# Kernel tuning notes

Hardware: AMD Instinct MI355X
Metric: run time of the kernel (lower is better)

The kernel has to match this reference:

```python
import jax, jax.numpy as jnp
import numpy as np

D_MODEL = 128
D_EDGE = 64


def setup_inputs() -> dict:
    key = jax.random.key(0)
    ks = jax.random.split(key, 12)
    B, N, E = 4, 50000, 600000
    x = jax.random.normal(ks[0], (B, N, D_MODEL), dtype=jnp.float32)
    edge_index = jax.random.randint(ks[1], (2, E), 0, N, dtype=jnp.int64)
    e_emb = jax.random.normal(ks[2], (E, D_EDGE), dtype=jnp.float32)
    batch_index = jax.random.randint(ks[3], (E,), 0, B, dtype=jnp.int64)
    s = 1.0 / np.sqrt(D_MODEL)
    se = 1.0 / np.sqrt(D_EDGE)
    Wq = jax.random.normal(ks[4], (D_MODEL, D_MODEL), dtype=jnp.float32) * s
    bq = jnp.zeros((D_MODEL,), dtype=jnp.float32)
    Wk = jax.random.normal(ks[5], (D_MODEL, D_MODEL), dtype=jnp.float32) * s
    bk = jnp.zeros((D_MODEL,), dtype=jnp.float32)
    Wv = jax.random.normal(ks[6], (D_MODEL, D_MODEL), dtype=jnp.float32) * s
    bv = jnp.zeros((D_MODEL,), dtype=jnp.float32)
    Wew = jax.random.normal(ks[7], (D_EDGE, D_MODEL), dtype=jnp.float32) * se
    bew = jnp.zeros((D_MODEL,), dtype=jnp.float32)
    Wev = jax.random.normal(ks[8], (D_EDGE, D_MODEL), dtype=jnp.float32) * se
    bev = jnp.zeros((D_MODEL,), dtype=jnp.float32)
    Wa = jax.random.normal(ks[9], (D_MODEL, 1), dtype=jnp.float32) * s
    return {"x": x, "edge_index": edge_index, "e_emb": e_emb,
            "batch_index": batch_index, "n_heads": 8,
            "Wq": Wq, "bq": bq, "Wk": Wk, "bk": bk, "Wv": Wv, "bv": bv,
            "Wew": Wew, "bew": bew, "Wev": Wev, "bev": bev, "Wa": Wa}


def reference(x, edge_index, e_emb, batch_index, n_heads,
              Wq, bq, Wk, bk, Wv, bv, Wew, bew, Wev, bev, Wa):
    B, N, d = x.shape
    d_h = d // n_heads
    Q = x @ Wq + bq          # [B, N, d]
    K = x @ Wk + bk
    V = x @ Wv + bv
    Ew = e_emb @ Wew + bew   # [E, d]
    Ev = e_emb @ Wev + bev
    src, dst = edge_index[0], edge_index[1]
    q_src = Q[batch_index, src, :]   # [E, d] gathers
    k_dst = K[batch_index, dst, :]
    v_dst = V[batch_index, dst, :]
    att_raw = q_src + k_dst + Ew
    att_logit = (att_raw @ Wa)[:, 0] / np.sqrt(d_h).astype(np.float32)
    att_exp = jnp.exp(att_logit)     # [E]
    group = batch_index * N + dst
    att_sum = jax.ops.segment_sum(att_exp, group, num_segments=B * N)
    alpha = att_exp / (att_sum[group] + 1e-9)
    msg = alpha[:, None] * (v_dst + Ev)          # [E, d]
    group_src = batch_index * N + src
    out_flat = jax.ops.segment_sum(msg, group_src, num_segments=B * N)
    return out_flat.reshape(B, N, d)
```

## Files before the change

kernel.cpp:

```cpp
#include <hip/hip_runtime.h>

#define DM 128
#define DE 64

static constexpr int kB = 4;
static constexpr int kN = 50000;
static constexpr int kE = 600000;
static constexpr int kNodes = kB * kN;

static constexpr size_t OFF_V    = 0;
static constexpr size_t OFF_T    = OFF_V + (size_t)kNodes * DM;
static constexpr size_t OFF_QA   = OFF_T + (size_t)kNodes * DE;
static constexpr size_t OFF_KA   = OFF_QA + kNodes;
static constexpr size_t OFF_ASUM = OFF_KA + kNodes;
static constexpr size_t OFF_CNT  = OFF_ASUM + kNodes;
static constexpr size_t OFF_AEXP = OFF_CNT + kNodes;
static constexpr size_t OFF_OFFS = OFF_AEXP + kE;
static constexpr size_t OFF_POS  = OFF_OFFS + kNodes;
static constexpr size_t OFF_BSUM = OFF_POS + kE;
static constexpr size_t OFF_BPRE = OFF_BSUM + 1024;
static constexpr size_t OFF_REC  = OFF_BPRE + 1024;
static constexpr size_t OFF_WQA  = OFF_REC + (size_t)kE * 4;
static constexpr size_t OFF_WKA  = OFF_WQA + DM;
static constexpr size_t OFF_WEWA = OFF_WKA + DM;
static constexpr size_t OFF_CB   = OFF_WEWA + DE;
static constexpr size_t OFF_WTH  = OFF_CB + 4;
static constexpr size_t OFF_WTL  = OFF_WTH + 8192;

static constexpr int kScanBlocks = (kNodes + 255) / 256;

typedef __attribute__((ext_vector_type(8))) short s8;
typedef __attribute__((ext_vector_type(4))) float f4;

__device__ inline void split2(float f, unsigned short& h, unsigned short& lo) {
  unsigned u = __float_as_uint(f);
  unsigned r = u + 0x7FFFu + ((u >> 16) & 1u);
  h = (unsigned short)(r >> 16);
  float fh = __uint_as_float((unsigned)h << 16);
  float d = f - fh;
  unsigned u2 = __float_as_uint(d);
  unsigned r2 = u2 + 0x7FFFu + ((u2 >> 16) & 1u);
  lo = (unsigned short)(r2 >> 16);
}

__global__ void k0_combine(const float* __restrict__ Wq, const float* __restrict__ Wk,
                           const float* __restrict__ Wew, const float* __restrict__ Wa,
                           const float* __restrict__ bq, const float* __restrict__ bk,
                           const float* __restrict__ bew, float* __restrict__ ws) {
  int t = threadIdx.x;
  if (t < DM) {
    float a = 0.f;
    for (int j = 0; j < DM; ++j) a += Wq[t * DM + j] * Wa[j];
    ws[OFF_WQA + t] = a;
  } else if (t < 2 * DM) {
    int i = t - DM;
    float a = 0.f;
    for (int j = 0; j < DM; ++j) a += Wk[i * DM + j] * Wa[j];
    ws[OFF_WKA + i] = a;
  } else if (t < 2 * DM + DE) {
    int i = t - 2 * DM;
    float a = 0.f;
    for (int j = 0; j < DM; ++j) a += Wew[i * DM + j] * Wa[j];
    ws[OFF_WEWA + i] = a;
  }
  if (t == 0) {
    float a = 0.f;
    for (int j = 0; j < DM; ++j) a += (bq[j] + bk[j] + bew[j]) * Wa[j];
    ws[OFF_CB] = a;
  }
}

__global__ __launch_bounds__(256) void k0b_wsplit(const float* __restrict__ Wv,
                                                  float* __restrict__ ws) {
  int idx = blockIdx.x * 256 + threadIdx.x;
  int j = idx & 127, k = idx >> 7;
  float w = Wv[k * DM + j];
  unsigned short hi, lo;
  split2(w, hi, lo);
  int kc = k & 31;
  int kp = (k & ~31) | (((kc >> 2) & 3) << 3) | ((kc >> 4) << 2) | (kc & 3);
  ((short*)(ws + OFF_WTH))[j * 128 + kp] = (short)hi;
  ((short*)(ws + OFF_WTL))[j * 128 + kp] = (short)lo;
}

__global__ __launch_bounds__(512) void k1_node(const float* __restrict__ x,
                                               const float* __restrict__ bv,
                                               float* __restrict__ ws) {
  __shared__ short xh[128][128];
  __shared__ short xl[128][128];
  __shared__ short wh[128][128];
  __shared__ short wl[128][128];
  const int t = threadIdx.x;
  const int row0 = blockIdx.x * 128;

  const short* wtgh = (const short*)(ws + OFF_WTH);
  const short* wtgl = (const short*)(ws + OFF_WTL);
  #pragma unroll
  for (int i = 0; i < 4; ++i) {
    int idx = t + i * 512;
    int j = idx >> 4;
    int c8 = (idx & 15) * 8;
    int col = (((c8 >> 3) ^ (j & 7)) << 3);
    *(int4*)&wh[j][col] = *(const int4*)(wtgh + j * 128 + c8);
    *(int4*)&wl[j][col] = *(const int4*)(wtgl + j * 128 + c8);
  }

  #pragma unroll
  for (int i = 0; i < 8; ++i) {
    int idx = t + i * 512;
    int r = idx >> 5;
    int c4 = (idx & 31) * 4;
    int rg = row0 + r; if (rg > kNodes - 1) rg = kNodes - 1;
    float4 v = *(const float4*)(x + (size_t)rg * DM + c4);
    unsigned short h0, h1, h2, h3, l0, l1, l2, l3;
    split2(v.x, h0, l0); split2(v.y, h1, l1);
    split2(v.z, h2, l2); split2(v.w, h3, l3);
    int kc = c4 & 31;
    int cp = (c4 & ~31) | (((kc >> 2) & 3) << 3) | ((kc >> 4) << 2);
    int col = ((((cp >> 3) ^ (r & 7)) << 3)) | (cp & 7);
    *(short4*)&xh[r][col] = make_short4((short)h0, (short)h1, (short)h2, (short)h3);
    *(short4*)&xl[r][col] = make_short4((short)l0, (short)l1, (short)l2, (short)l3);
  }

  if (t < 256) {
    int r = t & 127;
    int rg = row0 + r;
    if (rg < kNodes) {
      const float* wvec = (t < 128) ? (ws + OFF_WQA) : (ws + OFF_WKA);
      const float* xr = x + (size_t)rg * DM;
      float a = 0.f;
      #pragma unroll
      for (int k = 0; k < DM; k += 4) {
        float4 xv = *(const float4*)(xr + k);
        float4 wv = *(const float4*)(wvec + k);
        a += xv.x * wv.x + xv.y * wv.y + xv.z * wv.z + xv.w * wv.w;
      }
      ((t < 128) ? (ws + OFF_QA) : (ws + OFF_KA))[rg] = a;
    }
  }

  __syncthreads();

  const int l = t & 63;
  const int wid = t >> 6;
  const int wr = wid >> 1;
  const int wc = wid & 1;
  const int lrow = l & 15;
  const int lg = l >> 4;

  f4 acc[2][4];
  #pragma unroll
  for (int i = 0; i < 2; ++i)
    #pragma unroll
    for (int j = 0; j < 4; ++j) acc[i][j] = (f4){0.f, 0.f, 0.f, 0.f};

  #pragma unroll
  for (int ks = 0; ks < 4; ++ks) {
    s8 ah[2], al[2], bh[4], bl[4];
    #pragma unroll
    for (int i = 0; i < 2; ++i) {
      int r = wr * 32 + i * 16 + lrow;
      int col = (((ks * 4 + lg) ^ (r & 7)) << 3);
      ah[i] = *(const s8*)&xh[r][col];
      al[i] = *(const s8*)&xl[r][col];
    }
    #pragma unroll
    for (int j = 0; j < 4; ++j) {
      int r = wc * 64 + j * 16 + lrow;
      int col = (((ks * 4 + lg) ^ (r & 7)) << 3);
      bh[j] = *(const s8*)&wh[r][col];
      bl[j] = *(const s8*)&wl[r][col];
    }
    #pragma unroll
    for (int i = 0; i < 2; ++i)
      #pragma unroll
      for (int j = 0; j < 4; ++j) {
        acc[i][j] = __builtin_amdgcn_mfma_f32_16x16x32_bf16(ah[i], bh[j], acc[i][j], 0, 0, 0);
        acc[i][j] = __builtin_amdgcn_mfma_f32_16x16x32_bf16(ah[i], bl[j], acc[i][j], 0, 0, 0);
        acc[i][j] = __builtin_amdgcn_mfma_f32_16x16x32_bf16(al[i], bh[j], acc[i][j], 0, 0, 0);
      }
  }

  float* V = ws + OFF_V;
  #pragma unroll
  for (int i = 0; i < 2; ++i) {
    int rb = row0 + wr * 32 + i * 16 + lg * 4;
    #pragma unroll
    for (int j = 0; j < 4; ++j) {
      int colj = wc * 64 + j * 16 + lrow;
      float bvv = bv[colj];
      #pragma unroll
      for (int q = 0; q < 4; ++q) {
        int rr = rb + q;
        if (rr < kNodes) V[(size_t)rr * DM + colj] = acc[i][j][q] + bvv;
      }
    }
  }
}

__global__ __launch_bounds__(256) void k2_edge1(const int* __restrict__ ei,
                                                const int* __restrict__ bidx,
                                                const float* __restrict__ eemb,
                                                float* __restrict__ ws) {
  __shared__ float wewa_s[DE];
  __shared__ float cb_s;
  int t = threadIdx.x;
  if (t < DE) wewa_s[t] = ws[OFF_WEWA + t];
  if (t == DE) cb_s = ws[OFF_CB];
  __syncthreads();
  int e = blockIdx.x * 256 + t;
  if (e >= kE) return;
  int s = ei[e];
  int d = ei[kE + e];
  int b = bidx[e];
  const float4* emb = (const float4*)(eemb + (size_t)e * DE);
  float a = 0.f;
  #pragma unroll
  for (int i = 0; i < 16; ++i) {
    float4 v = emb[i];
    a += v.x * wewa_s[i * 4] + v.y * wewa_s[i * 4 + 1] +
         v.z * wewa_s[i * 4 + 2] + v.w * wewa_s[i * 4 + 3];
  }
  float logit = (ws[OFF_QA + b * kN + s] + ws[OFF_KA + b * kN + d] + a + cb_s) * 0.25f;
  float ex = __expf(logit);
  ws[OFF_AEXP + e] = ex;
  unsafeAtomicAdd(&ws[OFF_ASUM + b * kN + d], ex);
  int* wsi = (int*)ws;
  int gs = b * kN + s;
  wsi[OFF_POS + e] = atomicAdd(&wsi[OFF_CNT + gs], 1);
}

__global__ __launch_bounds__(256) void k_scan1(float* __restrict__ ws) {
  __shared__ int sh[256];
  int* wsi = (int*)ws;
  const int tid = threadIdx.x;
  const int i = blockIdx.x * 256 + tid;
  int v = (i < kNodes) ? wsi[OFF_CNT + i] : 0;
  int acc = v;
  sh[tid] = acc;
  __syncthreads();
  #pragma unroll
  for (int ofs = 1; ofs < 256; ofs <<= 1) {
    int add = (tid >= ofs) ? sh[tid - ofs] : 0;
    __syncthreads();
    acc += add;
    sh[tid] = acc;
    __syncthreads();
  }
  if (i < kNodes) wsi[OFF_OFFS + i] = acc - v;
  if (tid == 255) wsi[OFF_BSUM + blockIdx.x] = acc;
}

__global__ __launch_bounds__(1024) void k_scan2(float* __restrict__ ws) {
  __shared__ int sh[1024];
  int* wsi = (int*)ws;
  const int tid = threadIdx.x;
  int v = (tid < kScanBlocks) ? wsi[OFF_BSUM + tid] : 0;
  int acc = v;
  sh[tid] = acc;
  __syncthreads();
  for (int ofs = 1; ofs < 1024; ofs <<= 1) {
    int add = (tid >= ofs) ? sh[tid - ofs] : 0;
    __syncthreads();
    acc += add;
    sh[tid] = acc;
    __syncthreads();
  }
  wsi[OFF_BPRE + tid] = acc - v;
}

__global__ __launch_bounds__(256) void k_fill(const int* __restrict__ ei,
                                              const int* __restrict__ bidx,
                                              float* __restrict__ ws) {
  int e = blockIdx.x * 256 + threadIdx.x;
  if (e >= kE) return;
  int s = ei[e];
  int d = ei[kE + e];
  int b = bidx[e];
  int gs = b * kN + s;
  int gd = b * kN + d;
  const int* wsi = (const int*)ws;
  float alpha = ws[OFF_AEXP + e] / (ws[OFF_ASUM + gd] + 1e-9f);
  int p = wsi[OFF_OFFS + gs] + wsi[OFF_BPRE + (gs >> 8)] + wsi[OFF_POS + e];
  float4 r;
  r.x = alpha;
  r.y = __int_as_float(gd);
  r.z = __int_as_float(e);
  r.w = 0.f;
  ((float4*)(ws + OFF_REC))[p] = r;
}

__global__ __launch_bounds__(256) void k3_gather(const float* __restrict__ eemb,
                                                 const float* __restrict__ bev,
                                                 float* __restrict__ ws,
                                                 float* __restrict__ out) {
  const int lane = threadIdx.x & 63;
  const int g = (blockIdx.x * 256 + threadIdx.x) >> 6;
  if (g >= kNodes) return;
  const int* wsi = (const int*)ws;
  const float* V = ws + OFF_V;
  float* T = ws + OFF_T;
  const float4* rec = (const float4*)(ws + OFF_REC);
  const float bev0 = bev[lane];
  const float bev1 = bev[64 + lane];

  const int start = wsi[OFF_OFFS + g] + wsi[OFF_BPRE + (g >> 8)];
  const int deg = wsi[OFF_CNT + g];
  float o0 = 0.f, o1 = 0.f, tac = 0.f, ss = 0.f;
  for (int base = 0; base < deg; base += 4) {
    const int rem = deg - base;
    const int c1 = (rem > 1) ? 1 : 0;
    const int c2 = (rem > 2) ? 2 : c1;
    const int c3 = (rem > 3) ? 3 : c2;
    float4 r0 = rec[start + base];
    float4 r1 = rec[start + base + c1];
    float4 r2 = rec[start + base + c2];
    float4 r3 = rec[start + base + c3];
    float a0 = r0.x;
    float a1 = (rem > 1) ? r1.x : 0.f;
    float a2 = (rem > 2) ? r2.x : 0.f;
    float a3 = (rem > 3) ? r3.x : 0.f;
    const size_t gd0 = (size_t)__float_as_int(r0.y) * DM;
    const size_t gd1 = (size_t)__float_as_int(r1.y) * DM;
    const size_t gd2 = (size_t)__float_as_int(r2.y) * DM;
    const size_t gd3 = (size_t)__float_as_int(r3.y) * DM;
    const size_t e0 = (size_t)__float_as_int(r0.z) * DE;
    const size_t e1 = (size_t)__float_as_int(r1.z) * DE;
    const size_t e2 = (size_t)__float_as_int(r2.z) * DE;
    const size_t e3 = (size_t)__float_as_int(r3.z) * DE;
    float v00 = V[gd0 + lane],      v01 = V[gd1 + lane];
    float v02 = V[gd2 + lane],      v03 = V[gd3 + lane];
    float v10 = V[gd0 + 64 + lane], v11 = V[gd1 + 64 + lane];
    float v12 = V[gd2 + 64 + lane], v13 = V[gd3 + 64 + lane];
    float m0 = eemb[e0 + lane],     m1 = eemb[e1 + lane];
    float m2 = eemb[e2 + lane],     m3 = eemb[e3 + lane];
    o0 += a0 * v00 + a1 * v01 + a2 * v02 + a3 * v03;
    o1 += a0 * v10 + a1 * v11 + a2 * v12 + a3 * v13;
    tac += a0 * m0 + a1 * m1 + a2 * m2 + a3 * m3;
    ss += a0 + a1 + a2 + a3;
  }
  out[(size_t)g * DM + lane] = o0 + ss * bev0;
  out[(size_t)g * DM + 64 + lane] = o1 + ss * bev1;
  T[(size_t)g * DE + lane] = tac;
}

__global__ __launch_bounds__(256) void k4_wev(const float* __restrict__ Wev,
                                              float* __restrict__ ws,
                                              float* __restrict__ out) {
  __shared__ float ts[64][68];
  __shared__ float wes[64][132];
  const int t = threadIdx.x;
  const int row0 = blockIdx.x * 64;
  const float* T = ws + OFF_T;

  const float4* tg = (const float4*)(T + (size_t)row0 * DE);
  #pragma unroll
  for (int i = 0; i < 4; ++i) {
    int idx = t + i * 256;
    int r = idx >> 4, c = (idx & 15) * 4;
    *(float4*)&ts[r][c] = tg[idx];
  }
  const float4* wg = (const float4*)Wev;
  #pragma unroll
  for (int i = 0; i < 8; ++i) {
    int idx = t + i * 256;
    int r = idx >> 5, c = (idx & 31) * 4;
    *(float4*)&wes[r][c] = wg[idx];
  }
  __syncthreads();

  const int tx = t & 15, ty = t >> 4;
  const int j0 = tx * 8, r0 = ty * 4;
  float acc[4][8];
  #pragma unroll
  for (int i = 0; i < 4; ++i)
    #pragma unroll
    for (int j = 0; j < 8; ++j) acc[i][j] = 0.f;

  #pragma unroll
  for (int kk = 0; kk < DE; kk += 4) {
    float xv[4][4];
    #pragma unroll
    for (int i = 0; i < 4; ++i) {
      float4 tmp = *(const float4*)&ts[r0 + i][kk];
      xv[i][0] = tmp.x; xv[i][1] = tmp.y; xv[i][2] = tmp.z; xv[i][3] = tmp.w;
    }
    #pragma unroll
    for (int d = 0; d < 4; ++d) {
      float4 w0 = *(const float4*)&wes[kk + d][j0];
      float4 w1 = *(const float4*)&wes[kk + d][j0 + 4];
      float wj[8] = {w0.x, w0.y, w0.z, w0.w, w1.x, w1.y, w1.z, w1.w};
      #pragma unroll
      for (int i = 0; i < 4; ++i)
        #pragma unroll
        for (int j = 0; j < 8; ++j) acc[i][j] += xv[i][d] * wj[j];
    }
  }

  #pragma unroll
  for (int i = 0; i < 4; ++i) {
    size_t g = (size_t)(row0 + r0 + i);
    float4 o0 = *(const float4*)&out[g * DM + j0];
    float4 o1 = *(const float4*)&out[g * DM + j0 + 4];
    o0.x += acc[i][0]; o0.y += acc[i][1]; o0.z += acc[i][2]; o0.w += acc[i][3];
    o1.x += acc[i][4]; o1.y += acc[i][5]; o1.z += acc[i][6]; o1.w += acc[i][7];
    *(float4*)&out[g * DM + j0] = o0;
    *(float4*)&out[g * DM + j0 + 4] = o1;
  }
}

extern "C" void kernel_launch(void* const* d_in, const int* in_sizes, int n_in,
                              void* d_out, int out_size, void* d_ws, size_t ws_size,
                              hipStream_t stream) {
  const float* x    = (const float*)d_in[0];
  const int*   ei   = (const int*)d_in[1];
  const float* eemb = (const float*)d_in[2];
  const int*   bidx = (const int*)d_in[3];
  const float* Wq  = (const float*)d_in[5];
  const float* bq  = (const float*)d_in[6];
  const float* Wk  = (const float*)d_in[7];
  const float* bk  = (const float*)d_in[8];
  const float* Wv  = (const float*)d_in[9];
  const float* bv  = (const float*)d_in[10];
  const float* Wew = (const float*)d_in[11];
  const float* bew = (const float*)d_in[12];
  const float* Wev = (const float*)d_in[13];
  const float* bev = (const float*)d_in[14];
  const float* Wa  = (const float*)d_in[15];
  float* ws  = (float*)d_ws;
  float* out = (float*)d_out;

  hipMemsetAsync(ws + OFF_ASUM, 0, (size_t)2 * kNodes * sizeof(float), stream);

  k0_combine<<<1, 320, 0, stream>>>(Wq, Wk, Wew, Wa, bq, bk, bew, ws);
  k0b_wsplit<<<64, 256, 0, stream>>>(Wv, ws);
  k1_node<<<(kNodes + 127) / 128, 512, 0, stream>>>(x, bv, ws);
  k2_edge1<<<(kE + 255) / 256, 256, 0, stream>>>(ei, bidx, eemb, ws);
  k_scan1<<<kScanBlocks, 256, 0, stream>>>(ws);
  k_scan2<<<1, 1024, 0, stream>>>(ws);
  k_fill<<<(kE + 255) / 256, 256, 0, stream>>>(ei, bidx, ws);
  k3_gather<<<kNodes / 4, 256, 0, stream>>>(eemb, bev, ws, out);
  k4_wev<<<kNodes / 64, 256, 0, stream>>>(Wev, ws, out);
}
```

Measured before the change: 639.6 us.

## Fuse Wev projection into gather kernel via register-resident bf16 weights

Removes the separate k4_wev GEMM kernel and the T intermediate round-trip. The gather kernel now keeps Wev in registers as packed bf16 pairs, broadcasts each lane's accumulated edge-embedding sum with readlane, and applies the 64x128 projection before writing out. It also switches to a persistent grid-stride loop with 4096 blocks so the weight load is amortized. The cost is 64 extra VGPRs per thread, which may lower occupancy, 64 serial readlane+FMA steps per node, and bf16 rounding of Wev that reduces accuracy.

```diff
diff --git a/kernel.cpp b/kernel.cpp
--- a/kernel.cpp
+++ b/kernel.cpp
@@ -26,21 +26,23 @@
 static constexpr size_t OFF_CB   = OFF_WEWA + DE;
 static constexpr size_t OFF_WTH  = OFF_CB + 4;
 static constexpr size_t OFF_WTL  = OFF_WTH + 8192;
+static constexpr size_t OFF_WEVP = OFF_WTL + 8192;
 
 static constexpr int kScanBlocks = (kNodes + 255) / 256;
 
 typedef __attribute__((ext_vector_type(8))) short s8;
 typedef __attribute__((ext_vector_type(4))) float f4;
 
-__device__ inline void split2(float f, unsigned short& h, unsigned short& lo) {
+__device__ inline unsigned short bf16rne(float f) {
   unsigned u = __float_as_uint(f);
   unsigned r = u + 0x7FFFu + ((u >> 16) & 1u);
-  h = (unsigned short)(r >> 16);
+  return (unsigned short)(r >> 16);
+}
+
+__device__ inline void split2(float f, unsigned short& h, unsigned short& lo) {
+  h = bf16rne(f);
   float fh = __uint_as_float((unsigned)h << 16);
-  float d = f - fh;
-  unsigned u2 = __float_as_uint(d);
-  unsigned r2 = u2 + 0x7FFFu + ((u2 >> 16) & 1u);
-  lo = (unsigned short)(r2 >> 16);
+  lo = bf16rne(f - fh);
 }
 
 __global__ void k0_combine(const float* __restrict__ Wq, const float* __restrict__ Wk,
@@ -71,6 +73,7 @@
 }
 
 __global__ __launch_bounds__(256) void k0b_wsplit(const float* __restrict__ Wv,
+                                                  const float* __restrict__ Wev,
                                                   float* __restrict__ ws) {
   int idx = blockIdx.x * 256 + threadIdx.x;
   int j = idx & 127, k = idx >> 7;
@@ -81,6 +84,12 @@
   int kp = (k & ~31) | (((kc >> 2) & 3) << 3) | ((kc >> 4) << 2) | (kc & 3);
   ((short*)(ws + OFF_WTH))[j * 128 + kp] = (short)hi;
   ((short*)(ws + OFF_WTL))[j * 128 + kp] = (short)lo;
+  if (idx < 4096) {
+    int ke = idx >> 6, l = idx & 63;
+    unsigned a = bf16rne(Wev[ke * DM + l]);
+    unsigned b = bf16rne(Wev[ke * DM + 64 + l]);
+    ((unsigned*)(ws + OFF_WEVP))[idx] = a | (b << 16);
+  }
 }
 
 __global__ __launch_bounds__(512) void k1_node(const float* __restrict__ x,
@@ -295,117 +304,66 @@
                                                  float* __restrict__ ws,
                                                  float* __restrict__ out) {
   const int lane = threadIdx.x & 63;
-  const int g = (blockIdx.x * 256 + threadIdx.x) >> 6;
-  if (g >= kNodes) return;
+  const int gw = (blockIdx.x * 256 + threadIdx.x) >> 6;
+  const int nw = (gridDim.x * 256) >> 6;
   const int* wsi = (const int*)ws;
   const float* V = ws + OFF_V;
-  float* T = ws + OFF_T;
   const float4* rec = (const float4*)(ws + OFF_REC);
   const float bev0 = bev[lane];
   const float bev1 = bev[64 + lane];
 
-  const int start = wsi[OFF_OFFS + g] + wsi[OFF_BPRE + (g >> 8)];
-  const int deg = wsi[OFF_CNT + g];
-  float o0 = 0.f, o1 = 0.f, tac = 0.f, ss = 0.f;
-  for (int base = 0; base < deg; base += 4) {
-    const int rem = deg - base;
-    const int c1 = (rem > 1) ? 1 : 0;
-    const int c2 = (rem > 2) ? 2 : c1;
-    const int c3 = (rem > 3) ? 3 : c2;
-    float4 r0 = rec[start + base];
-    float4 r1 = rec[start + base + c1];
-    float4 r2 = rec[start + base + c2];
-    float4 r3 = rec[start + base + c3];
-    float a0 = r0.x;
-    float a1 = (rem > 1) ? r1.x : 0.f;
-    float a2 = (rem > 2) ? r2.x : 0.f;
-    float a3 = (rem > 3) ? r3.x : 0.f;
-    const size_t gd0 = (size_t)__float_as_int(r0.y) * DM;
-    const size_t gd1 = (size_t)__float_as_int(r1.y) * DM;
-    const size_t gd2 = (size_t)__float_as_int(r2.y) * DM;
-    const size_t gd3 = (size_t)__float_as_int(r3.y) * DM;
-    const size_t e0 = (size_t)__float_as_int(r0.z) * DE;
-    const size_t e1 = (size_t)__float_as_int(r1.z) * DE;
-    const size_t e2 = (size_t)__float_as_int(r2.z) * DE;
-    const size_t e3 = (size_t)__float_as_int(r3.z) * DE;
-    float v00 = V[gd0 + lane],      v01 = V[gd1 + lane];
-    float v02 = V[gd2 + lane],      v03 = V[gd3 + lane];
-    float v10 = V[gd0 + 64 + lane], v11 = V[gd1 + 64 + lane];
-    float v12 = V[gd2 + 64 + lane], v13 = V[gd3 + 64 + lane];
-    float m0 = eemb[e0 + lane],     m1 = eemb[e1 + lane];
-    float m2 = eemb[e2 + lane],     m3 = eemb[e3 + lane];
-    o0 += a0 * v00 + a1 * v01 + a2 * v02 + a3 * v03;
-    o1 += a0 * v10 + a1 * v11 + a2 * v12 + a3 * v13;
-    tac += a0 * m0 + a1 * m1 + a2 * m2 + a3 * m3;
-    ss += a0 + a1 + a2 + a3;
-  }
-  out[(size_t)g * DM + lane] = o0 + ss * bev0;
-  out[(size_t)g * DM + 64 + lane] = o1 + ss * bev1;
-  T[(size_t)g * DE + lane] = tac;
-}
-
-__global__ __launch_bounds__(256) void k4_wev(const float* __restrict__ Wev,
-                                              float* __restrict__ ws,
-                                              float* __restrict__ out) {
-  __shared__ float ts[64][68];
-  __shared__ float wes[64][132];
-  const int t = threadIdx.x;
-  const int row0 = blockIdx.x * 64;
-  const float* T = ws + OFF_T;
-
-  const float4* tg = (const float4*)(T + (size_t)row0 * DE);
-  #pragma unroll
-  for (int i = 0; i < 4; ++i) {
-    int idx = t + i * 256;
-    int r = idx >> 4, c = (idx & 15) * 4;
-    *(float4*)&ts[r][c] = tg[idx];
-  }
-  const float4* wg = (const float4*)Wev;
-  #pragma unroll
-  for (int i = 0; i < 8; ++i) {
-    int idx = t + i * 256;
-    int r = idx >> 5, c = (idx & 31) * 4;
-    *(float4*)&wes[r][c] = wg[idx];
-  }
-  __syncthreads();
-
-  const int tx = t & 15, ty = t >> 4;
-  const int j0 = tx * 8, r0 = ty * 4;
-  float acc[4][8];
-  #pragma unroll
-  for (int i = 0; i < 4; ++i)
-    #pragma unroll
-    for (int j = 0; j < 8; ++j) acc[i][j] = 0.f;
-
-  #pragma unroll
-  for (int kk = 0; kk < DE; kk += 4) {
-    float xv[4][4];
-    #pragma unroll
-    for (int i = 0; i < 4; ++i) {
-      float4 tmp = *(const float4*)&ts[r0 + i][kk];
-      xv[i][0] = tmp.x; xv[i][1] = tmp.y; xv[i][2] = tmp.z; xv[i][3] = tmp.w;
-    }
-    #pragma unroll
-    for (int d = 0; d < 4; ++d) {
-      float4 w0 = *(const float4*)&wes[kk + d][j0];
-      float4 w1 = *(const float4*)&wes[kk + d][j0 + 4];
-      float wj[8] = {w0.x, w0.y, w0.z, w0.w, w1.x, w1.y, w1.z, w1.w};
-      #pragma unroll
-      for (int i = 0; i < 4; ++i)
-        #pragma unroll
-        for (int j = 0; j < 8; ++j) acc[i][j] += xv[i][d] * wj[j];
-    }
-  }
-
-  #pragma unroll
-  for (int i = 0; i < 4; ++i) {
-    size_t g = (size_t)(row0 + r0 + i);
-    float4 o0 = *(const float4*)&out[g * DM + j0];
-    float4 o1 = *(const float4*)&out[g * DM + j0 + 4];
-    o0.x += acc[i][0]; o0.y += acc[i][1]; o0.z += acc[i][2]; o0.w += acc[i][3];
-    o1.x += acc[i][4]; o1.y += acc[i][5]; o1.z += acc[i][6]; o1.w += acc[i][7];
-    *(float4*)&out[g * DM + j0] = o0;
-    *(float4*)&out[g * DM + j0 + 4] = o1;
+  const unsigned* wevpg = (const unsigned*)(ws + OFF_WEVP);
+  unsigned wevp[64];
+  #pragma unroll
+  for (int k = 0; k < 64; ++k) wevp[k] = wevpg[k * 64 + lane];
+
+  for (int g = gw; g < kNodes; g += nw) {
+    const int start = wsi[OFF_OFFS + g] + wsi[OFF_BPRE + (g >> 8)];
+    const int deg = wsi[OFF_CNT + g];
+    float o0 = 0.f, o1 = 0.f, tac = 0.f, ss = 0.f;
+    for (int base = 0; base < deg; base += 4) {
+      const int rem = deg - base;
+      const int c1 = (rem > 1) ? 1 : 0;
+      const int c2 = (rem > 2) ? 2 : c1;
+      const int c3 = (rem > 3) ? 3 : c2;
+      float4 r0 = rec[start + base];
+      float4 r1 = rec[start + base + c1];
+      float4 r2 = rec[start + base + c2];
+      float4 r3 = rec[start + base + c3];
+      float a0 = r0.x;
+      float a1 = (rem > 1) ? r1.x : 0.f;
+      float a2 = (rem > 2) ? r2.x : 0.f;
+      float a3 = (rem > 3) ? r3.x : 0.f;
+      const size_t gd0 = (size_t)__float_as_int(r0.y) * DM;
+      const size_t gd1 = (size_t)__float_as_int(r1.y) * DM;
+      const size_t gd2 = (size_t)__float_as_int(r2.y) * DM;
+      const size_t gd3 = (size_t)__float_as_int(r3.y) * DM;
+      const size_t e0 = (size_t)__float_as_int(r0.z) * DE;
+      const size_t e1 = (size_t)__float_as_int(r1.z) * DE;
+      const size_t e2 = (size_t)__float_as_int(r2.z) * DE;
+      const size_t e3 = (size_t)__float_as_int(r3.z) * DE;
+      float v00 = V[gd0 + lane],      v01 = V[gd1 + lane];
+      float v02 = V[gd2 + lane],      v03 = V[gd3 + lane];
+      float v10 = V[gd0 + 64 + lane], v11 = V[gd1 + 64 + lane];
+      float v12 = V[gd2 + 64 + lane], v13 = V[gd3 + 64 + lane];
+      float m0 = eemb[e0 + lane],     m1 = eemb[e1 + lane];
+      float m2 = eemb[e2 + lane],     m3 = eemb[e3 + lane];
+      o0 += a0 * v00 + a1 * v01 + a2 * v02 + a3 * v03;
+      o1 += a0 * v10 + a1 * v11 + a2 * v12 + a3 * v13;
+      tac += a0 * m0 + a1 * m1 + a2 * m2 + a3 * m3;
+      ss += a0 + a1 + a2 + a3;
+    }
+    float res0 = o0 + ss * bev0;
+    float res1 = o1 + ss * bev1;
+    #pragma unroll
+    for (int k = 0; k < 64; ++k) {
+      float tk = __int_as_float(__builtin_amdgcn_readlane(__float_as_int(tac), k));
+      unsigned p = wevp[k];
+      res0 = fmaf(tk, __uint_as_float(p << 16), res0);
+      res1 = fmaf(tk, __uint_as_float(p & 0xFFFF0000u), res1);
+    }
+    out[(size_t)g * DM + lane] = res0;
+    out[(size_t)g * DM + 64 + lane] = res1;
   }
 }
 
@@ -433,12 +391,11 @@
   hipMemsetAsync(ws + OFF_ASUM, 0, (size_t)2 * kNodes * sizeof(float), stream);
 
   k0_combine<<<1, 320, 0, stream>>>(Wq, Wk, Wew, Wa, bq, bk, bew, ws);
-  k0b_wsplit<<<64, 256, 0, stream>>>(Wv, ws);
+  k0b_wsplit<<<64, 256, 0, stream>>>(Wv, Wev, ws);
   k1_node<<<(kNodes + 127) / 128, 512, 0, stream>>>(x, bv, ws);
   k2_edge1<<<(kE + 255) / 256, 256, 0, stream>>>(ei, bidx, eemb, ws);
   k_scan1<<<kScanBlocks, 256, 0, stream>>>(ws);
   k_scan2<<<1, 1024, 0, stream>>>(ws);
   k_fill<<<(kE + 255) / 256, 256, 0, stream>>>(ei, bidx, ws);
-  k3_gather<<<kNodes / 4, 256, 0, stream>>>(eemb, bev, ws, out);
-  k4_wev<<<kNodes / 64, 256, 0, stream>>>(Wev, ws, out);
-}
+  k3_gather<<<4096, 256, 0, stream>>>(eemb, bev, ws, out);
+}
```

New measurement: 733.2 us. 14.6% more time.
